# Performance work log

Hardware: AMD Instinct MI355X
Metric: run time of the kernel (lower is better)

The kernel has to match this reference:

```python
import jax, jax.numpy as jnp
import numpy as np

N_NODES = 100000
N_EDGES = 1600000
D_FEAT = 128
HIDDEN = 256


def setup_inputs() -> dict:
    key = jax.random.key(0)
    k1, k2, k3, k4, k5, k6, k7 = jax.random.split(key, 7)
    h = jax.random.normal(k1, (N_NODES, D_FEAT), dtype=jnp.float32)
    src = jax.random.randint(k2, (N_EDGES,), 0, N_NODES, dtype=jnp.int64)
    dst = jax.random.randint(k3, (N_EDGES,), 0, N_NODES, dtype=jnp.int64)
    # Linear weights, torch layout: W [out, in], b [out]
    lim1 = 1.0 / np.sqrt(2 * D_FEAT)
    W1_w = jax.random.uniform(k4, (HIDDEN, 2 * D_FEAT), minval=-lim1, maxval=lim1, dtype=jnp.float32)
    W1_b = jax.random.uniform(k5, (HIDDEN,), minval=-lim1, maxval=lim1, dtype=jnp.float32)
    lim2 = 1.0 / np.sqrt(HIDDEN)
    W2_w = jax.random.uniform(k6, (1, HIDDEN), minval=-lim2, maxval=lim2, dtype=jnp.float32)
    W2_b = jax.random.uniform(k7, (1,), minval=-lim2, maxval=lim2, dtype=jnp.float32)
    return {"h": h, "src": src, "dst": dst, "W1_w": W1_w, "W1_b": W1_b, "W2_w": W2_w, "W2_b": W2_b}


def reference(h, src, dst, W1_w, W1_b, W2_w, W2_b):
    # gather per-edge src/dst node features and concat: [E, 2D]
    x = jnp.concatenate([h[src], h[dst]], axis=1)
    # Linear -> ReLU -> Linear, squeeze last dim -> [E]
    hid = jax.nn.relu(x @ W1_w.T + W1_b)          # [E, H]
    score = (hid @ W2_w.T + W2_b)[:, 0]           # [E]
    return score
```

## Files before the change

### kernel.cpp

```cpp
#include <hip/hip_runtime.h>


#define NNODES 100000
#define E_TOTAL 1600000
#define D 128
#define K2 256
#define H 256

typedef short bf16x8 __attribute__((ext_vector_type(8)));
typedef short bf16x4 __attribute__((ext_vector_type(4)));
typedef float f32x4 __attribute__((ext_vector_type(4)));
typedef const __attribute__((address_space(1))) unsigned short* gas_t;
typedef __attribute__((address_space(3))) unsigned short* las_t;

#if defined(__has_attribute)
#if __has_attribute(amdgpu_waves_per_eu)
#define LB __launch_bounds__(256) __attribute__((amdgpu_waves_per_eu(2, 2)))
#else
#define LB __launch_bounds__(256, 2)
#endif
#else
#define LB __launch_bounds__(256, 2)
#endif

__device__ __forceinline__ unsigned short f2bf(float f) {
    unsigned u = __float_as_uint(f);
    u += 0x7fff + ((u >> 16) & 1);
    return (unsigned short)(u >> 16);
}
__device__ __forceinline__ float bf2f(unsigned short s) {
    return __uint_as_float((unsigned)s << 16);
}


__global__ LB void u_gemm(
    const float* __restrict__ h,
    const float* __restrict__ W1,
    const float* __restrict__ b1,
    unsigned short* __restrict__ Us,
    unsigned short* __restrict__ Ud)
{
    __shared__ __align__(16) unsigned short A[64 * 136];

    const int tid = threadIdx.x;
    const int wave = tid >> 6;
    const int lane = tid & 63;
    const int l15 = lane & 15;
    const int quad = lane >> 4;

    const int r0 = blockIdx.x * 64;
    int rows = NNODES - r0; if (rows > 64) rows = 64;

    const float4* hf4 = (const float4*)(h + (size_t)r0 * D);
    const int lim = rows * 32;
#pragma unroll
    for (int i = 0; i < 8; ++i) {
        int j = tid + i * 256;
        if (j < lim) {
            float4 v = hf4[j];
            bf16x4 b;
            b[0] = (short)f2bf(v.x); b[1] = (short)f2bf(v.y);
            b[2] = (short)f2bf(v.z); b[3] = (short)f2bf(v.w);
            *(bf16x4*)&A[(j >> 5) * 136 + (j & 31) * 4] = b;
        }
    }
    __syncthreads();

#pragma unroll
    for (int half = 0; half < 2; ++half) {
        const int koff = half * 128;
        unsigned short* U = half ? Ud : Us;

        bf16x8 B[4][4];
        float bias[4];
#pragma unroll
        for (int nt = 0; nt < 4; ++nt) {
            const int n = wave * 64 + nt * 16 + l15;
            bias[nt] = half ? 0.f : b1[n];
#pragma unroll
            for (int kit = 0; kit < 4; ++kit) {
                const float* wp = W1 + (size_t)n * K2 + koff + kit * 32 + quad * 8;
                float4 x = *(const float4*)wp;
                float4 y = *(const float4*)(wp + 4);
                bf16x8 f;
                f[0] = (short)f2bf(x.x); f[1] = (short)f2bf(x.y);
                f[2] = (short)f2bf(x.z); f[3] = (short)f2bf(x.w);
                f[4] = (short)f2bf(y.x); f[5] = (short)f2bf(y.y);
                f[6] = (short)f2bf(y.z); f[7] = (short)f2bf(y.w);
                B[kit][nt] = f;
            }
        }

        f32x4 acc[4][4];
        const f32x4 zero = {0.f, 0.f, 0.f, 0.f};
#pragma unroll
        for (int ms = 0; ms < 4; ++ms)
#pragma unroll
            for (int nt = 0; nt < 4; ++nt)
                acc[ms][nt] = zero;

#pragma unroll
        for (int kit = 0; kit < 4; ++kit) {
            bf16x8 a[4];
#pragma unroll
            for (int ms = 0; ms < 4; ++ms)
                a[ms] = *(const bf16x8*)&A[(ms * 16 + l15) * 136 + kit * 32 + quad * 8];
#pragma unroll
            for (int ms = 0; ms < 4; ++ms)
#pragma unroll
                for (int nt = 0; nt < 4; ++nt)
                    acc[ms][nt] = __builtin_amdgcn_mfma_f32_16x16x32_bf16(
                        a[ms], B[kit][nt], acc[ms][nt], 0, 0, 0);
        }

#pragma unroll
        for (int ms = 0; ms < 4; ++ms) {
#pragma unroll
            for (int r = 0; r < 4; ++r) {
                const int m = ms * 16 + quad * 4 + r;
                if (m < rows) {
                    unsigned short* rowp = U + (size_t)(r0 + m) * H + wave * 64;
#pragma unroll
                    for (int nt = 0; nt < 4; ++nt)
                        rowp[nt * 16 + l15] = f2bf(acc[ms][nt][r] + bias[nt]);
                }
            }
        }
    }
}

__global__ __launch_bounds__(256) void edge_score(
    const unsigned short* __restrict__ Us,
    const unsigned short* __restrict__ Ud,
    const int* __restrict__ srcE,
    const int* __restrict__ dstE,
    const float* __restrict__ w2,
    const float* __restrict__ b2p,
    float* __restrict__ out)
{
    const int gt = blockIdx.x * 256 + threadIdx.x;
    const int l = gt & 15;
    const int q = gt >> 4;
    const int Q = (gridDim.x * 256) >> 4;

    float w2v[16];
#pragma unroll
    for (int j = 0; j < 16; ++j) w2v[j] = w2[l * 16 + j];
    const float b2 = *b2p;

    for (int e = q; e < E_TOTAL; e += Q) {
        const int s = srcE[e];
        const int d = dstE[e];
        const bf16x8* us = (const bf16x8*)(Us + (size_t)s * H + l * 16);
        const bf16x8* ud = (const bf16x8*)(Ud + (size_t)d * H + l * 16);
        bf16x8 u0 = us[0], u1 = us[1];
        bf16x8 v0 = ud[0], v1 = ud[1];

        float acc = 0.f;
#pragma unroll
        for (int j = 0; j < 8; ++j) {
            float hv = bf2f((unsigned short)u0[j]) + bf2f((unsigned short)v0[j]);
            acc = fmaf(fmaxf(hv, 0.f), w2v[j], acc);
        }
#pragma unroll
        for (int j = 0; j < 8; ++j) {
            float hv = bf2f((unsigned short)u1[j]) + bf2f((unsigned short)v1[j]);
            acc = fmaf(fmaxf(hv, 0.f), w2v[j + 8], acc);
        }
        acc += __shfl_xor(acc, 1, 16);
        acc += __shfl_xor(acc, 2, 16);
        acc += __shfl_xor(acc, 4, 16);
        acc += __shfl_xor(acc, 8, 16);
        if (l == 0) out[e] = acc + b2;
    }
}


#define TILE_M 32
#define NTILES (E_TOTAL / TILE_M)
#define GRID 2500

__global__ void cvt_kernel(const float* __restrict__ h, const float* __restrict__ w1,
                           unsigned short* __restrict__ hbf, unsigned short* __restrict__ w1bf,
                           int n4h, int n4w) {
    int i = blockIdx.x * blockDim.x + threadIdx.x;
    const float* s; unsigned short* d; int j;
    if (i < n4h) { s = h; d = hbf; j = i; }
    else if (i < n4h + n4w) { s = w1; d = w1bf; j = i - n4h; }
    else return;
    float4 v = ((const float4*)s)[j];
    ushort4 o;
    o.x = f2bf(v.x); o.y = f2bf(v.y); o.z = f2bf(v.z); o.w = f2bf(v.w);
    ((ushort4*)d)[j] = o;
}

__global__ LB void edge_mlp(
    const unsigned short* __restrict__ hbf,
    const int* __restrict__ srcE,
    const int* __restrict__ dstE,
    const unsigned short* __restrict__ w1bf,
    const float* __restrict__ b1,
    const float* __restrict__ w2,
    const float* __restrict__ b2p,
    float* __restrict__ out)
{
    __shared__ __align__(16) unsigned short X[2][TILE_M * K2];
    __shared__ float red[2][TILE_M][5];

    const int tid = threadIdx.x;
    const int wave = tid >> 6;
    const int lane = tid & 63;
    const int lane15 = lane & 15;
    const int quad = lane >> 4;

    bf16x8 B[8][4];
#pragma unroll
    for (int kit = 0; kit < 8; ++kit)
#pragma unroll
        for (int nt = 0; nt < 4; ++nt) {
            int n = wave * 64 + nt * 16 + lane15;
            int k = kit * 32 + quad * 8;
            B[kit][nt] = *(const bf16x8*)(w1bf + n * K2 + k);
        }

    float b1v[4], w2v[4];
#pragma unroll
    for (int nt = 0; nt < 4; ++nt) {
        int n = wave * 64 + nt * 16 + lane15;
        b1v[nt] = b1[n];
        w2v[nt] = w2[n];
    }
    const float b2 = *b2p;

    const int r_off = tid >> 5;
    const int c = (tid & 31) ^ (r_off & 7);
    const int half = c >> 4;
    const int fc = c & 15;
    const int* idx_base = half ? dstE : srcE;
    const int gshort = fc * 8;

    const int t0 = blockIdx.x;
    int inode[4];

#pragma unroll
    for (int it = 0; it < 4; ++it)
        inode[it] = idx_base[t0 * TILE_M + it * 8 + r_off];
#pragma unroll
    for (int it = 0; it < 4; ++it)
        __builtin_amdgcn_global_load_lds(
            (gas_t)(hbf + inode[it] * D + gshort),
            (las_t)(&X[0][0] + it * 2048 + wave * 512), 16, 0, 0);
    {
        const int t1 = t0 + GRID;
#pragma unroll
        for (int it = 0; it < 4; ++it)
            inode[it] = idx_base[t1 * TILE_M + it * 8 + r_off];
    }

    int buf = 0;
    int prev_eb = -1;

    for (int tile = t0; tile < NTILES; tile += GRID) {
        __syncthreads();

        const int nt1 = tile + GRID;
        if (nt1 < NTILES) {
            unsigned short* Xn = &X[buf ^ 1][0];
#pragma unroll
            for (int it = 0; it < 4; ++it)
                __builtin_amdgcn_global_load_lds(
                    (gas_t)(hbf + inode[it] * D + gshort),
                    (las_t)(Xn + it * 2048 + wave * 512), 16, 0, 0);
        }
        const int nt2 = tile + 2 * GRID;
        if (nt2 < NTILES) {
            const int eb2 = nt2 * TILE_M;
#pragma unroll
            for (int it = 0; it < 4; ++it)
                inode[it] = idx_base[eb2 + it * 8 + r_off];
        }
        if (prev_eb >= 0 && tid < TILE_M) {
            float s = b2;
#pragma unroll
            for (int w = 0; w < 4; ++w) s += red[buf ^ 1][tid][w];
            out[prev_eb + tid] = s;
        }

        const unsigned short* Xc = &X[buf][0];
        f32x4 acc[2][4];
        const f32x4 zero = {0.f, 0.f, 0.f, 0.f};
#pragma unroll
        for (int ms = 0; ms < 2; ++ms)
#pragma unroll
            for (int nt = 0; nt < 4; ++nt)
                acc[ms][nt] = zero;

#pragma unroll
        for (int kit = 0; kit < 8; ++kit) {
            const int p8 = (((kit * 4 + quad) ^ (lane15 & 7))) * 8;
            bf16x8 a[2];
#pragma unroll
            for (int ms = 0; ms < 2; ++ms)
                a[ms] = *(const bf16x8*)&Xc[(ms * 16 + lane15) * K2 + p8];
#pragma unroll
            for (int ms = 0; ms < 2; ++ms)
#pragma unroll
                for (int nt = 0; nt < 4; ++nt)
                    acc[ms][nt] = __builtin_amdgcn_mfma_f32_16x16x32_bf16(
                        a[ms], B[kit][nt], acc[ms][nt], 0, 0, 0);
        }

#pragma unroll
        for (int ms = 0; ms < 2; ++ms)
#pragma unroll
            for (int r = 0; r < 4; ++r) {
                float p = 0.f;
#pragma unroll
                for (int nt = 0; nt < 4; ++nt) {
                    float hv = acc[ms][nt][r] + b1v[nt];
                    p = fmaf(fmaxf(hv, 0.f), w2v[nt], p);
                }
                p += __shfl_xor(p, 1, 16);
                p += __shfl_xor(p, 2, 16);
                p += __shfl_xor(p, 4, 16);
                p += __shfl_xor(p, 8, 16);
                if (lane15 == 0) red[buf][ms * 16 + quad * 4 + r][wave] = p;
            }
        prev_eb = tile * TILE_M;
        buf ^= 1;
    }

    __syncthreads();
    if (prev_eb >= 0 && tid < TILE_M) {
        float s = b2;
#pragma unroll
        for (int w = 0; w < 4; ++w) s += red[buf ^ 1][tid][w];
        out[prev_eb + tid] = s;
    }
}


extern "C" void kernel_launch(void* const* d_in, const int* in_sizes, int n_in,
                              void* d_out, int out_size, void* d_ws, size_t ws_size,
                              hipStream_t stream) {
    const float* h    = (const float*)d_in[0];
    const int*   srcE = (const int*)d_in[1];
    const int*   dstE = (const int*)d_in[2];
    const float* W1   = (const float*)d_in[3];
    const float* b1   = (const float*)d_in[4];
    const float* w2   = (const float*)d_in[5];
    const float* b2   = (const float*)d_in[6];
    float* out = (float*)d_out;

    const size_t planeElems = (size_t)NNODES * H;
    const size_t need = planeElems * 2 * sizeof(unsigned short);

    if (ws_size >= need) {
        unsigned short* Us = (unsigned short*)d_ws;
        unsigned short* Ud = Us + planeElems;
        u_gemm<<<(NNODES + 63) / 64, 256, 0, stream>>>(h, W1, b1, Us, Ud);
        edge_score<<<4096, 256, 0, stream>>>(Us, Ud, srcE, dstE, w2, b2, out);
    } else {
        unsigned short* hbf  = (unsigned short*)d_ws;
        unsigned short* w1bf = hbf + (size_t)NNODES * D;
        int n4h = NNODES * D / 4;
        int n4w = H * K2 / 4;
        int n4 = n4h + n4w;
        cvt_kernel<<<(n4 + 255) / 256, 256, 0, stream>>>(h, W1, hbf, w1bf, n4h, n4w);
        edge_mlp<<<GRID, 256, 0, stream>>>(hbf, srcE, dstE, w1bf, b1, w2, b2, out);
    }
}
```

Measured before the change: 394.5 us.

## Stage GEMM output through LDS for coalesced stores; batch four edges per group

The node GEMM now writes its bf16 results into a padded shared-memory tile and then copies whole rows to global memory with 16-byte stores, replacing the scattered 2-byte stores. The edge scoring kernel handles four edges per 16-lane group, using vector loads for the indices, issuing all eight gathers before any math, and writing four scores with one float4 store. This is meant to raise memory-level parallelism and cut store transactions, at the cost of more registers and extra LDS plus barriers in the GEMM kernel. Only the u_gemm and edge_score paths change, and it is unclear which kernels are actually launched.

```diff
diff --git a/kernel.cpp b/kernel.cpp
--- a/kernel.cpp
+++ b/kernel.cpp
@@ -13,16 +13,6 @@
 typedef const __attribute__((address_space(1))) unsigned short* gas_t;
 typedef __attribute__((address_space(3))) unsigned short* las_t;
 
-#if defined(__has_attribute)
-#if __has_attribute(amdgpu_waves_per_eu)
-#define LB __launch_bounds__(256) __attribute__((amdgpu_waves_per_eu(2, 2)))
-#else
-#define LB __launch_bounds__(256, 2)
-#endif
-#else
-#define LB __launch_bounds__(256, 2)
-#endif
-
 __device__ __forceinline__ unsigned short f2bf(float f) {
     unsigned u = __float_as_uint(f);
     u += 0x7fff + ((u >> 16) & 1);
@@ -33,7 +23,7 @@
 }
 
 
-__global__ LB void u_gemm(
+__global__ __launch_bounds__(256, 2) void u_gemm(
     const float* __restrict__ h,
     const float* __restrict__ W1,
     const float* __restrict__ b1,
@@ -41,6 +31,7 @@
     unsigned short* __restrict__ Ud)
 {
     __shared__ __align__(16) unsigned short A[64 * 136];
+    __shared__ __align__(16) unsigned short S[64 * 268];
 
     const int tid = threadIdx.x;
     const int wave = tid >> 6;
@@ -66,7 +57,6 @@
     }
     __syncthreads();
 
-#pragma unroll
     for (int half = 0; half < 2; ++half) {
         const int koff = half * 128;
         unsigned short* U = half ? Ud : Us;
@@ -113,17 +103,27 @@
                         a[ms], B[kit][nt], acc[ms][nt], 0, 0, 0);
         }
 
-#pragma unroll
-        for (int ms = 0; ms < 4; ++ms) {
+        if (half) __syncthreads();
+#pragma unroll
+        for (int ms = 0; ms < 4; ++ms)
 #pragma unroll
             for (int r = 0; r < 4; ++r) {
                 const int m = ms * 16 + quad * 4 + r;
-                if (m < rows) {
-                    unsigned short* rowp = U + (size_t)(r0 + m) * H + wave * 64;
-#pragma unroll
-                    for (int nt = 0; nt < 4; ++nt)
-                        rowp[nt * 16 + l15] = f2bf(acc[ms][nt][r] + bias[nt]);
-                }
+#pragma unroll
+                for (int nt = 0; nt < 4; ++nt)
+                    S[m * 268 + wave * 64 + nt * 16 + l15] =
+                        f2bf(acc[ms][nt][r] + bias[nt]);
+            }
+        __syncthreads();
+
+#pragma unroll
+        for (int i = 0; i < 8; ++i) {
+            const int j = i * 256 + tid;
+            const int row = j >> 5;
+            const int cc = j & 31;
+            if (row < rows) {
+                bf16x8 vv = *(const bf16x8*)&S[row * 268 + cc * 8];
+                *(bf16x8*)(U + (size_t)(r0 + row) * H + cc * 8) = vv;
             }
         }
     }
@@ -142,36 +142,51 @@
     const int l = gt & 15;
     const int q = gt >> 4;
     const int Q = (gridDim.x * 256) >> 4;
+    const int NGRP = E_TOTAL / 4;
 
     float w2v[16];
 #pragma unroll
     for (int j = 0; j < 16; ++j) w2v[j] = w2[l * 16 + j];
     const float b2 = *b2p;
 
-    for (int e = q; e < E_TOTAL; e += Q) {
-        const int s = srcE[e];
-        const int d = dstE[e];
-        const bf16x8* us = (const bf16x8*)(Us + (size_t)s * H + l * 16);
-        const bf16x8* ud = (const bf16x8*)(Ud + (size_t)d * H + l * 16);
-        bf16x8 u0 = us[0], u1 = us[1];
-        bf16x8 v0 = ud[0], v1 = ud[1];
-
-        float acc = 0.f;
-#pragma unroll
-        for (int j = 0; j < 8; ++j) {
-            float hv = bf2f((unsigned short)u0[j]) + bf2f((unsigned short)v0[j]);
-            acc = fmaf(fmaxf(hv, 0.f), w2v[j], acc);
-        }
-#pragma unroll
-        for (int j = 0; j < 8; ++j) {
-            float hv = bf2f((unsigned short)u1[j]) + bf2f((unsigned short)v1[j]);
-            acc = fmaf(fmaxf(hv, 0.f), w2v[j + 8], acc);
-        }
-        acc += __shfl_xor(acc, 1, 16);
-        acc += __shfl_xor(acc, 2, 16);
-        acc += __shfl_xor(acc, 4, 16);
-        acc += __shfl_xor(acc, 8, 16);
-        if (l == 0) out[e] = acc + b2;
+    for (int g = q; g < NGRP; g += Q) {
+        const int e0 = g * 4;
+        const int4 s4 = *(const int4*)(srcE + e0);
+        const int4 d4 = *(const int4*)(dstE + e0);
+        const int sv[4] = {s4.x, s4.y, s4.z, s4.w};
+        const int dv[4] = {d4.x, d4.y, d4.z, d4.w};
+
+        bf16x8 u[4][2], v[4][2];
+#pragma unroll
+        for (int k = 0; k < 4; ++k) {
+            const bf16x8* us = (const bf16x8*)(Us + (size_t)sv[k] * H + l * 16);
+            const bf16x8* ud = (const bf16x8*)(Ud + (size_t)dv[k] * H + l * 16);
+            u[k][0] = us[0]; u[k][1] = us[1];
+            v[k][0] = ud[0]; v[k][1] = ud[1];
+        }
+
+        float4 res;
+        float* resp = (float*)&res;
+#pragma unroll
+        for (int k = 0; k < 4; ++k) {
+            float acc = 0.f;
+#pragma unroll
+            for (int j = 0; j < 8; ++j) {
+                float hv = bf2f((unsigned short)u[k][0][j]) + bf2f((unsigned short)v[k][0][j]);
+                acc = fmaf(fmaxf(hv, 0.f), w2v[j], acc);
+            }
+#pragma unroll
+            for (int j = 0; j < 8; ++j) {
+                float hv = bf2f((unsigned short)u[k][1][j]) + bf2f((unsigned short)v[k][1][j]);
+                acc = fmaf(fmaxf(hv, 0.f), w2v[j + 8], acc);
+            }
+            acc += __shfl_xor(acc, 1, 16);
+            acc += __shfl_xor(acc, 2, 16);
+            acc += __shfl_xor(acc, 4, 16);
+            acc += __shfl_xor(acc, 8, 16);
+            resp[k] = acc + b2;
+        }
+        if (l == 0) *(float4*)(out + e0) = res;
     }
 }
 
@@ -179,6 +194,16 @@
 #define TILE_M 32
 #define NTILES (E_TOTAL / TILE_M)
 #define GRID 2500
+
+#if defined(__has_attribute)
+#if __has_attribute(amdgpu_waves_per_eu)
+#define LB __launch_bounds__(256) __attribute__((amdgpu_waves_per_eu(2, 2)))
+#else
+#define LB __launch_bounds__(256, 2)
+#endif
+#else
+#define LB __launch_bounds__(256, 2)
+#endif
 
 __global__ void cvt_kernel(const float* __restrict__ h, const float* __restrict__ w1,
                            unsigned short* __restrict__ hbf, unsigned short* __restrict__ w1bf,
```

New measurement: 385.1 us. -2.4%, faster.
